# Kernel tuning notes

Measured on AMD Instinct MI355X. Metric: run time of the kernel, lower is better.

Reference implementation:

```python
import jax, jax.numpy as jnp
import numpy as np

B, S, D = 8, 512, 256          # batch, seq_len, input_depth
E, H = 8, 4                    # num_experts, num_heads
DK = DV = DO = 256             # total_key/value/output depth (per expert)
DH = DK // H                   # head dim = 64
SCALE = DH ** -0.5


def setup_inputs() -> dict:
    key = jax.random.key(0)
    ks = jax.random.split(key, 8)
    queries = jax.random.normal(ks[0], (B, S, D), jnp.float32)
    keys = jax.random.normal(ks[1], (B, S, D), jnp.float32)
    values = jax.random.normal(ks[2], (B, S, D), jnp.float32)
    mask = jax.random.randint(ks[3], (B, S, S), 0, 2).astype(bool)
    s = 0.05
    Wq = jax.random.normal(ks[4], (D, DK * E), jnp.float32) * s
    Wk = jax.random.normal(ks[5], (D, DK * E), jnp.float32) * s
    Wv = jax.random.normal(ks[6], (D, DV * E), jnp.float32) * s
    Wo = jax.random.normal(ks[7], (DV, DO * E), jnp.float32) * s
    return {"queries": queries, "keys": keys, "values": values, "mask": mask,
            "Wq": Wq, "Wk": Wk, "Wv": Wv, "Wo": Wo}


def _split_heads(x):
    # [B, S, E*H*DH] -> [B, E, H, S, DH]
    b, s, _ = x.shape
    return x.reshape(b, s, E, H, -1).transpose(0, 2, 3, 1, 4)


def reference(queries, keys, values, mask, Wq, Wk, Wv, Wo):
    q = _split_heads(queries @ Wq) * SCALE   # [B,E,H,S,DH]
    k = _split_heads(keys @ Wk)
    v = _split_heads(values @ Wv)
    logits = jnp.einsum('behqd,behkd->behqk', q, k)      # [B,E,H,S,S]
    m = mask[:, None, None].astype(jnp.float32)          # [B,1,1,S,S]
    logits = logits * (1.0 - m) + (-1e18) * m
    w = jax.nn.softmax(logits, axis=-1)
    ctx = jnp.einsum('behqk,behkd->behqd', w, v)         # [B,E,H,S,DH]
    # merge heads -> [B, S, E, H*DH]
    ctx = ctx.transpose(0, 3, 1, 2, 4).reshape(B, S, E, H * DH)
    # faithful quirk: Dense applied on rank-4 tensor -> [B,S,E,DO*E]
    return ctx @ Wo
```

## Files before the change

### kernel.cpp

```cpp
#include <hip/hip_runtime.h>
#include <stdint.h>


typedef __bf16 bf16x8 __attribute__((ext_vector_type(8)));
typedef float f32x4 __attribute__((ext_vector_type(4)));
typedef unsigned short u16x8 __attribute__((ext_vector_type(8)));
typedef unsigned short u16x4 __attribute__((ext_vector_type(4)));

#define MFMA16(a, b, c) __builtin_amdgcn_mfma_f32_16x16x32_bf16(a, b, c, 0, 0, 0)

__device__ __forceinline__ unsigned short f2bf(float x) {
    uint32_t u = __builtin_bit_cast(uint32_t, x);
    u += 0x7FFFu + ((u >> 16) & 1u);
    return (unsigned short)(u >> 16);
}

__global__ __launch_bounds__(256) void prep_kern(
        const float* __restrict__ q, const float* __restrict__ k,
        const float* __restrict__ v, const int* __restrict__ mask,
        const float* __restrict__ Wq, const float* __restrict__ Wk,
        const float* __restrict__ Wv, const float* __restrict__ Wo,
        unsigned short* __restrict__ qb, unsigned short* __restrict__ kb,
        unsigned short* __restrict__ vb, unsigned short* __restrict__ wt,
        uint32_t* __restrict__ maskbits) {
    __shared__ float tile[32][33];
    const int x = blockIdx.x, t = threadIdx.x;
    if (x < 3072) {
        int which = x >> 10;
        const float* s = (which == 0) ? q : (which == 1) ? k : v;
        unsigned short* o = (which == 0) ? qb : (which == 1) ? kb : vb;
        int i = ((x & 1023) * 256 + t) * 4;
        float4 f = *(const float4*)&s[i];
        u16x4 r;
        r[0] = f2bf(f.x); r[1] = f2bf(f.y); r[2] = f2bf(f.z); r[3] = f2bf(f.w);
        *(u16x4*)&o[i] = r;
    } else if (x < 5120) {
        int y = x - 3072;
        int wsel = y >> 9;
        const float* W = (wsel == 0) ? Wq : (wsel == 1) ? Wk : (wsel == 2) ? Wv : Wo;
        unsigned short* T = wt + wsel * 2048 * 256;
        int rem = y & 511;
        int c0 = (rem & 63) * 32, r0 = (rem >> 6) * 32;
        int tr = t >> 3, tc = (t & 7) * 4;
        float4 f = *(const float4*)&W[(r0 + tr) * 2048 + c0 + tc];
        tile[tr][tc + 0] = f.x; tile[tr][tc + 1] = f.y;
        tile[tr][tc + 2] = f.z; tile[tr][tc + 3] = f.w;
        __syncthreads();
        u16x4 o;
        o[0] = f2bf(tile[tc + 0][tr]); o[1] = f2bf(tile[tc + 1][tr]);
        o[2] = f2bf(tile[tc + 2][tr]); o[3] = f2bf(tile[tc + 3][tr]);
        *(u16x4*)&T[(c0 + tr) * 256 + r0 + tc] = o;
    } else {
        int wdx = (x - 5120) * 256 + t;
        int b = wdx >> 13, kt = (wdx >> 9) & 15, row = wdx & 511;
        const int4* mp = (const int4*)(mask + ((size_t)(b * 512 + row)) * 512 + kt * 32);
        uint32_t word = 0;
#pragma unroll
        for (int j = 0; j < 8; ++j) {
            int4 m4 = mp[j];
            word |= (uint32_t)(m4.x != 0) << (j * 4 + 0);
            word |= (uint32_t)(m4.y != 0) << (j * 4 + 1);
            word |= (uint32_t)(m4.z != 0) << (j * 4 + 2);
            word |= (uint32_t)(m4.w != 0) << (j * 4 + 3);
        }
        maskbits[wdx] = word;
    }
}

__global__ __launch_bounds__(512) void fused_kern(
        const unsigned short* __restrict__ actq,
        const unsigned short* __restrict__ actk,
        const unsigned short* __restrict__ actv,
        const unsigned short* __restrict__ Wt,
        const uint32_t* __restrict__ maskbits,
        unsigned short* __restrict__ CTX) {
    __shared__ unsigned short Klds[512 * 64];
    __shared__ unsigned short Vt[64 * 512];
    __shared__ unsigned short R3[64 * 128];
    const int bid = (int)blockIdx.x;
    const int flat = (bid & 7) * 32 + (bid >> 3);
    const int b = flat >> 5, eh = flat & 31;
    const int e = eh >> 2, h = eh & 3;
    const int t = threadIdx.x, w = t >> 6, l = t & 63, li = l & 15, g = l >> 4;
    const int tw0 = w * 64;
    const size_t actoff = (size_t)b * 512 * 256;
    const size_t wso = ((size_t)(e * 256 + h * 64)) * 256;

    bf16x8 qf[4][2];

    for (int p = 0; p < 3; ++p) {
        const unsigned short* A = ((p == 0) ? actq : (p == 1) ? actk : actv) + actoff;
        const unsigned short* W = Wt + (size_t)p * 2048 * 256 + wso;
        f32x4 acc[4][4];
#pragma unroll
        for (int m = 0; m < 4; ++m)
#pragma unroll
            for (int n = 0; n < 4; ++n) acc[m][n] = (f32x4){0.f, 0.f, 0.f, 0.f};
        for (int kh = 0; kh < 2; ++kh) {
            __syncthreads();
#pragma unroll
            for (int j = 0; j < 2; ++j) {
                int c = t + j * 512;
                int nr = c >> 4, k8 = (c & 15) * 8;
                *(u16x8*)&R3[nr * 128 + (k8 ^ ((nr & 7) << 3))] =
                    *(const u16x8*)&W[(size_t)nr * 256 + kh * 128 + k8];
            }
            __syncthreads();
#pragma unroll
            for (int kk = 0; kk < 4; ++kk) {
                const int k0 = kh * 128 + kk * 32;
                bf16x8 af[4], bfr[4];
#pragma unroll
                for (int m = 0; m < 4; ++m)
                    af[m] = *(const bf16x8*)&A[(size_t)(tw0 + m * 16 + li) * 256 + k0 + g * 8];
#pragma unroll
                for (int n = 0; n < 4; ++n) {
                    int nr = n * 16 + li;
                    bfr[n] = *(const bf16x8*)&R3[nr * 128 + ((kk * 32 + g * 8) ^ ((nr & 7) << 3))];
                }
                if (p == 2) {
#pragma unroll
                    for (int m = 0; m < 4; ++m)
#pragma unroll
                        for (int n = 0; n < 4; ++n)
                            acc[m][n] = MFMA16(af[m], bfr[n], acc[m][n]);
                } else {
#pragma unroll
                    for (int m = 0; m < 4; ++m)
#pragma unroll
                        for (int n = 0; n < 4; ++n)
                            acc[m][n] = MFMA16(bfr[n], af[m], acc[m][n]);
                }
            }
        }
        if (p == 0) {
            unsigned short* qs = Klds + w * 4096;
#pragma unroll
            for (int m = 0; m < 4; ++m)
#pragma unroll
                for (int n = 0; n < 4; ++n) {
                    int row = m * 16 + li, dh = n * 16 + g * 4;
                    u16x4 o;
#pragma unroll
                    for (int i = 0; i < 4; ++i) o[i] = f2bf(acc[m][n][i] * 0.125f);
                    *(u16x4*)&qs[row * 64 + (dh ^ ((row & 7) << 3))] = o;
                }
#pragma unroll
            for (int m = 0; m < 4; ++m) {
                int row = m * 16 + li;
                qf[m][0] = *(const bf16x8*)&qs[row * 64 + ((g * 8) ^ ((row & 7) << 3))];
                qf[m][1] = *(const bf16x8*)&qs[row * 64 + ((32 + g * 8) ^ ((row & 7) << 3))];
            }
        } else if (p == 1) {
#pragma unroll
            for (int m = 0; m < 4; ++m)
#pragma unroll
                for (int n = 0; n < 4; ++n) {
                    int tok = tw0 + m * 16 + li, dh = n * 16 + g * 4;
                    u16x4 o;
#pragma unroll
                    for (int i = 0; i < 4; ++i) o[i] = f2bf(acc[m][n][i]);
                    *(u16x4*)&Klds[tok * 64 + (dh ^ (((tok >> 1) & 7) << 3))] = o;
                }
        } else {
#pragma unroll
            for (int m = 0; m < 4; ++m)
#pragma unroll
                for (int n = 0; n < 4; ++n) {
                    int tok = tw0 + m * 16 + g * 4, dh = n * 16 + li;
                    u16x4 o;
#pragma unroll
                    for (int i = 0; i < 4; ++i) o[i] = f2bf(acc[m][n][i]);
                    *(u16x4*)&Vt[dh * 512 + (tok ^ ((dh & 7) << 3))] = o;
                }
        }
    }
    __syncthreads();

    bf16x8 vaug;
#pragma unroll
    for (int j = 0; j < 8; ++j) vaug[j] = (li == 0) ? (__bf16)1.0f : (__bf16)0.0f;
    f32x4 atc[4][4], lacc[4];
#pragma unroll
    for (int m = 0; m < 4; ++m) {
#pragma unroll
        for (int c = 0; c < 4; ++c) atc[m][c] = (f32x4){0.f, 0.f, 0.f, 0.f};
        lacc[m] = (f32x4){0.f, 0.f, 0.f, 0.f};
    }
    unsigned short* Pw = R3 + w * 1024;

    for (int kt = 0; kt < 16; ++kt) {
        bf16x8 kf[2][2];
#pragma unroll
        for (int f = 0; f < 2; ++f) {
            int tok = kt * 32 + 2 * li + f;
            const unsigned short* kr = &Klds[tok * 64];
            int sw = ((tok >> 1) & 7) << 3;
            kf[f][0] = *(const bf16x8*)&kr[(g * 8) ^ sw];
            kf[f][1] = *(const bf16x8*)&kr[(32 + g * 8) ^ sw];
        }
        f32x4 s[4][2];
#pragma unroll
        for (int m = 0; m < 4; ++m)
#pragma unroll
            for (int f = 0; f < 2; ++f) {
                f32x4 zz = (f32x4){0.f, 0.f, 0.f, 0.f};
                zz = MFMA16(qf[m][0], kf[f][0], zz);
                zz = MFMA16(qf[m][1], kf[f][1], zz);
                s[m][f] = zz;
            }
#pragma unroll
        for (int m = 0; m < 4; ++m) {
            const uint4 mw = *(const uint4*)&maskbits[(size_t)(b * 16 + kt) * 512 +
                                                      w * 64 + m * 16 + g * 4];
#pragma unroll
            for (int i = 0; i < 4; ++i) {
                uint32_t word = (i == 0) ? mw.x : (i == 1) ? mw.y : (i == 2) ? mw.z : mw.w;
                uint32_t pair = (word >> (2 * li)) & 3u;
                if (pair & 1u) s[m][0][i] = -20.f;
                if (pair & 2u) s[m][1][i] = -20.f;
            }
        }
        bf16x8 bv[4];
#pragma unroll
        for (int c = 0; c < 4; ++c) {
            int dh = c * 16 + li;
            bv[c] = *(const bf16x8*)&Vt[dh * 512 + ((kt * 32 + g * 8) ^ ((dh & 7) << 3))];
        }
#pragma unroll
        for (int mh = 0; mh < 2; ++mh) {
#pragma unroll
            for (int mm = 0; mm < 2; ++mm) {
                int m = mh * 2 + mm;
#pragma unroll
                for (int i = 0; i < 4; ++i) {
                    int row = mm * 16 + g * 4 + i;
                    uint32_t pk = (uint32_t)f2bf(__expf(s[m][0][i])) |
                                  ((uint32_t)f2bf(__expf(s[m][1][i])) << 16);
                    *(uint32_t*)&Pw[row * 32 + ((2 * li) ^ ((row & 3) << 3))] = pk;
                }
            }
#pragma unroll
            for (int mm = 0; mm < 2; ++mm) {
                int m = mh * 2 + mm;
                int rm = mm * 16 + li;
                bf16x8 pa = *(const bf16x8*)&Pw[rm * 32 + ((g * 8) ^ ((rm & 3) << 3))];
#pragma unroll
                for (int c = 0; c < 4; ++c)
                    atc[m][c] = MFMA16(bv[c], pa, atc[m][c]);
                lacc[m] = MFMA16(vaug, pa, lacc[m]);
            }
        }
    }
#pragma unroll
    for (int m = 0; m < 4; ++m) {
        float l_i = __shfl(lacc[m][0], l & 15, 64);
        float inv = 1.0f / l_i;
        const int qrow = w * 64 + m * 16 + li;
#pragma unroll
        for (int c = 0; c < 4; ++c) {
            u16x4 o;
#pragma unroll
            for (int i = 0; i < 4; ++i) o[i] = f2bf(atc[m][c][i] * inv);
            *(u16x4*)&CTX[(size_t)((b * 512 + qrow) * 8 + e) * 256 +
                          h * 64 + c * 16 + g * 4] = o;
        }
    }
}

__global__ __launch_bounds__(256) void gemm_kern(
        const unsigned short* __restrict__ A,
        const unsigned short* __restrict__ Bt,
        float* __restrict__ C, int cpx) {
    __shared__ unsigned short Asl[128 * 72];
    __shared__ unsigned short Bsl[128 * 72];
    const int bid = (int)blockIdx.x;
    const int logical = (bid & 7) * cpx + (bid >> 3);
    const int bx = logical & 15;
    const int by = logical >> 4;
    const int t = threadIdx.x, l = t & 63, w = t >> 6;
    const int li = l & 15, g = l >> 4;
    const int wr = w >> 1, wc = w & 1;
    const int rowA = by * 128, colB = bx * 128;
    f32x4 acc[4][4];
#pragma unroll
    for (int m = 0; m < 4; ++m)
#pragma unroll
        for (int n = 0; n < 4; ++n) acc[m][n] = (f32x4){0.f, 0.f, 0.f, 0.f};

    for (int kk = 0; kk < 4; ++kk) {
#pragma unroll
        for (int j = 0; j < 4; ++j) {
            int chunk = t + j * 256;
            int row = chunk >> 3, c8 = (chunk & 7) * 8;
            *(u16x8*)&Asl[row * 72 + c8] =
                *(const u16x8*)&A[(size_t)(rowA + row) * 256 + kk * 64 + c8];
            *(u16x8*)&Bsl[row * 72 + c8] =
                *(const u16x8*)&Bt[(size_t)(colB + row) * 256 + kk * 64 + c8];
        }
        __syncthreads();
#pragma unroll
        for (int hh = 0; hh < 2; ++hh) {
            bf16x8 af[4], bfr[4];
#pragma unroll
            for (int m = 0; m < 4; ++m)
                af[m] = *(const bf16x8*)&Asl[(wr * 64 + m * 16 + li) * 72 + hh * 32 + g * 8];
#pragma unroll
            for (int n = 0; n < 4; ++n)
                bfr[n] = *(const bf16x8*)&Bsl[(wc * 64 + n * 16 + li) * 72 + hh * 32 + g * 8];
#pragma unroll
            for (int m = 0; m < 4; ++m)
#pragma unroll
                for (int n = 0; n < 4; ++n)
                    acc[m][n] = MFMA16(bfr[n], af[m], acc[m][n]);
        }
        __syncthreads();
    }
#pragma unroll
    for (int m = 0; m < 4; ++m) {
        const int r = rowA + wr * 64 + m * 16 + li;
#pragma unroll
        for (int n = 0; n < 4; ++n) {
            const int c = colB + wc * 64 + n * 16 + g * 4;
            __builtin_nontemporal_store(acc[m][n], (f32x4*)&C[(size_t)r * 2048 + c]);
        }
    }
}

extern "C" void kernel_launch(void* const* d_in, const int* in_sizes, int n_in,
                              void* d_out, int out_size, void* d_ws, size_t ws_size,
                              hipStream_t stream) {
    (void)in_sizes; (void)n_in; (void)out_size; (void)ws_size;
    const float* queries = (const float*)d_in[0];
    const float* keys    = (const float*)d_in[1];
    const float* values  = (const float*)d_in[2];
    const int*   mask    = (const int*)d_in[3];
    const float* Wq = (const float*)d_in[4];
    const float* Wk = (const float*)d_in[5];
    const float* Wv = (const float*)d_in[6];
    const float* Wo = (const float*)d_in[7];

    unsigned short* CTX = (unsigned short*)d_ws;
    unsigned short* Qbf = CTX + (size_t)32768 * 256;
    unsigned short* Wt  = Qbf + (size_t)3 * 4096 * 256;
    uint32_t* maskbits  = (uint32_t*)(Wt + (size_t)4 * 2048 * 256);

    prep_kern<<<dim3(5376), 256, 0, stream>>>(queries, keys, values, mask,
                                              Wq, Wk, Wv, Wo,
                                              Qbf, Qbf + 4096 * 256, Qbf + 2 * 4096 * 256,
                                              Wt, maskbits);
    fused_kern<<<dim3(256), 512, 0, stream>>>(Qbf, Qbf + 4096 * 256,
                                              Qbf + 2 * 4096 * 256,
                                              Wt, maskbits, CTX);
    gemm_kern<<<dim3(4096), 256, 0, stream>>>(CTX, Wt + (size_t)3 * 2048 * 256,
                                              (float*)d_out, 512);
}
```

Before: 162.6 us.

## Double fused attention block to 1024 threads, use exp2 softmax and hardware bf16 cast

The fused projection+attention kernel now runs 16 waves per block, each owning 32 query/token rows instead of 64. This halves per-wave accumulator state and spreads the MFMA work over more waves to improve latency hiding. Softmax now uses exp2 with log2e folded into the Q scale and the mask constant. The manual round-to-nearest bf16 conversion is replaced by the compiler's native bf16 cast. Risks are register pressure under the 1024-thread launch bound and the extra barrier cost of the larger block.

```diff
diff --git a/kernel.cpp b/kernel.cpp
--- a/kernel.cpp
+++ b/kernel.cpp
@@ -9,11 +9,13 @@
 
 #define MFMA16(a, b, c) __builtin_amdgcn_mfma_f32_16x16x32_bf16(a, b, c, 0, 0, 0)
 
-__device__ __forceinline__ unsigned short f2bf(float x) {
-    uint32_t u = __builtin_bit_cast(uint32_t, x);
-    u += 0x7FFFu + ((u >> 16) & 1u);
-    return (unsigned short)(u >> 16);
-}
+__device__ __forceinline__ unsigned short bfc(float x) {
+    __bf16 b = (__bf16)x;
+    return __builtin_bit_cast(unsigned short, b);
+}
+
+#define QSCALE 0.18033688011112042f
+#define MASKVAL -28.853900817779268f
 
 __global__ __launch_bounds__(256) void prep_kern(
         const float* __restrict__ q, const float* __restrict__ k,
@@ -32,7 +34,7 @@
         int i = ((x & 1023) * 256 + t) * 4;
         float4 f = *(const float4*)&s[i];
         u16x4 r;
-        r[0] = f2bf(f.x); r[1] = f2bf(f.y); r[2] = f2bf(f.z); r[3] = f2bf(f.w);
+        r[0] = bfc(f.x); r[1] = bfc(f.y); r[2] = bfc(f.z); r[3] = bfc(f.w);
         *(u16x4*)&o[i] = r;
     } else if (x < 5120) {
         int y = x - 3072;
@@ -47,8 +49,8 @@
         tile[tr][tc + 2] = f.z; tile[tr][tc + 3] = f.w;
         __syncthreads();
         u16x4 o;
-        o[0] = f2bf(tile[tc + 0][tr]); o[1] = f2bf(tile[tc + 1][tr]);
-        o[2] = f2bf(tile[tc + 2][tr]); o[3] = f2bf(tile[tc + 3][tr]);
+        o[0] = bfc(tile[tc + 0][tr]); o[1] = bfc(tile[tc + 1][tr]);
+        o[2] = bfc(tile[tc + 2][tr]); o[3] = bfc(tile[tc + 3][tr]);
         *(u16x4*)&T[(c0 + tr) * 256 + r0 + tc] = o;
     } else {
         int wdx = (x - 5120) * 256 + t;
@@ -67,7 +69,7 @@
     }
 }
 
-__global__ __launch_bounds__(512) void fused_kern(
+__global__ __launch_bounds__(1024) void fused_kern(
         const unsigned short* __restrict__ actq,
         const unsigned short* __restrict__ actk,
         const unsigned short* __restrict__ actv,
@@ -82,26 +84,24 @@
     const int b = flat >> 5, eh = flat & 31;
     const int e = eh >> 2, h = eh & 3;
     const int t = threadIdx.x, w = t >> 6, l = t & 63, li = l & 15, g = l >> 4;
-    const int tw0 = w * 64;
+    const int tw0 = w * 32;
     const size_t actoff = (size_t)b * 512 * 256;
     const size_t wso = ((size_t)(e * 256 + h * 64)) * 256;
 
-    bf16x8 qf[4][2];
+    bf16x8 qf[2][2];
 
     for (int p = 0; p < 3; ++p) {
         const unsigned short* A = ((p == 0) ? actq : (p == 1) ? actk : actv) + actoff;
         const unsigned short* W = Wt + (size_t)p * 2048 * 256 + wso;
-        f32x4 acc[4][4];
-#pragma unroll
-        for (int m = 0; m < 4; ++m)
+        f32x4 acc[2][4];
+#pragma unroll
+        for (int m = 0; m < 2; ++m)
 #pragma unroll
             for (int n = 0; n < 4; ++n) acc[m][n] = (f32x4){0.f, 0.f, 0.f, 0.f};
         for (int kh = 0; kh < 2; ++kh) {
             __syncthreads();
-#pragma unroll
-            for (int j = 0; j < 2; ++j) {
-                int c = t + j * 512;
-                int nr = c >> 4, k8 = (c & 15) * 8;
+            {
+                int nr = t >> 4, k8 = (t & 15) * 8;
                 *(u16x8*)&R3[nr * 128 + (k8 ^ ((nr & 7) << 3))] =
                     *(const u16x8*)&W[(size_t)nr * 256 + kh * 128 + k8];
             }
@@ -109,9 +109,9 @@
 #pragma unroll
             for (int kk = 0; kk < 4; ++kk) {
                 const int k0 = kh * 128 + kk * 32;
-                bf16x8 af[4], bfr[4];
-#pragma unroll
-                for (int m = 0; m < 4; ++m)
+                bf16x8 af[2], bfr[4];
+#pragma unroll
+                for (int m = 0; m < 2; ++m)
                     af[m] = *(const bf16x8*)&A[(size_t)(tw0 + m * 16 + li) * 256 + k0 + g * 8];
 #pragma unroll
                 for (int n = 0; n < 4; ++n) {
@@ -120,13 +120,13 @@
                 }
                 if (p == 2) {
 #pragma unroll
-                    for (int m = 0; m < 4; ++m)
+                    for (int m = 0; m < 2; ++m)
 #pragma unroll
                         for (int n = 0; n < 4; ++n)
                             acc[m][n] = MFMA16(af[m], bfr[n], acc[m][n]);
                 } else {
 #pragma unroll
-                    for (int m = 0; m < 4; ++m)
+                    for (int m = 0; m < 2; ++m)
 #pragma unroll
                         for (int n = 0; n < 4; ++n)
                             acc[m][n] = MFMA16(bfr[n], af[m], acc[m][n]);
@@ -134,43 +134,43 @@
             }
         }
         if (p == 0) {
-            unsigned short* qs = Klds + w * 4096;
-#pragma unroll
-            for (int m = 0; m < 4; ++m)
+            unsigned short* qs = Klds + w * 2048;
+#pragma unroll
+            for (int m = 0; m < 2; ++m)
 #pragma unroll
                 for (int n = 0; n < 4; ++n) {
                     int row = m * 16 + li, dh = n * 16 + g * 4;
                     u16x4 o;
 #pragma unroll
-                    for (int i = 0; i < 4; ++i) o[i] = f2bf(acc[m][n][i] * 0.125f);
+                    for (int i = 0; i < 4; ++i) o[i] = bfc(acc[m][n][i] * QSCALE);
                     *(u16x4*)&qs[row * 64 + (dh ^ ((row & 7) << 3))] = o;
                 }
 #pragma unroll
-            for (int m = 0; m < 4; ++m) {
+            for (int m = 0; m < 2; ++m) {
                 int row = m * 16 + li;
                 qf[m][0] = *(const bf16x8*)&qs[row * 64 + ((g * 8) ^ ((row & 7) << 3))];
                 qf[m][1] = *(const bf16x8*)&qs[row * 64 + ((32 + g * 8) ^ ((row & 7) << 3))];
             }
         } else if (p == 1) {
 #pragma unroll
-            for (int m = 0; m < 4; ++m)
+            for (int m = 0; m < 2; ++m)
 #pragma unroll
                 for (int n = 0; n < 4; ++n) {
                     int tok = tw0 + m * 16 + li, dh = n * 16 + g * 4;
                     u16x4 o;
 #pragma unroll
-                    for (int i = 0; i < 4; ++i) o[i] = f2bf(acc[m][n][i]);
+                    for (int i = 0; i < 4; ++i) o[i] = bfc(acc[m][n][i]);
                     *(u16x4*)&Klds[tok * 64 + (dh ^ (((tok >> 1) & 7) << 3))] = o;
                 }
         } else {
 #pragma unroll
-            for (int m = 0; m < 4; ++m)
+            for (int m = 0; m < 2; ++m)
 #pragma unroll
                 for (int n = 0; n < 4; ++n) {
                     int tok = tw0 + m * 16 + g * 4, dh = n * 16 + li;
                     u16x4 o;
 #pragma unroll
-                    for (int i = 0; i < 4; ++i) o[i] = f2bf(acc[m][n][i]);
+                    for (int i = 0; i < 4; ++i) o[i] = bfc(acc[m][n][i]);
                     *(u16x4*)&Vt[dh * 512 + (tok ^ ((dh & 7) << 3))] = o;
                 }
         }
@@ -180,14 +180,15 @@
     bf16x8 vaug;
 #pragma unroll
     for (int j = 0; j < 8; ++j) vaug[j] = (li == 0) ? (__bf16)1.0f : (__bf16)0.0f;
-    f32x4 atc[4][4], lacc[4];
-#pragma unroll
-    for (int m = 0; m < 4; ++m) {
+    f32x4 atc[2][4], lacc[2];
+#pragma unroll
+    for (int m = 0; m < 2; ++m) {
 #pragma unroll
         for (int c = 0; c < 4; ++c) atc[m][c] = (f32x4){0.f, 0.f, 0.f, 0.f};
         lacc[m] = (f32x4){0.f, 0.f, 0.f, 0.f};
     }
-    unsigned short* Pw = R3 + w * 1024;
+    unsigned short* Pw = R3 + w * 512;
+    const uint32_t* mb = maskbits + (size_t)b * 16 * 512;
 
     for (int kt = 0; kt < 16; ++kt) {
         bf16x8 kf[2][2];
@@ -199,9 +200,9 @@
             kf[f][0] = *(const bf16x8*)&kr[(g * 8) ^ sw];
             kf[f][1] = *(const bf16x8*)&kr[(32 + g * 8) ^ sw];
         }
-        f32x4 s[4][2];
-#pragma unroll
-        for (int m = 0; m < 4; ++m)
+        f32x4 s[2][2];
+#pragma unroll
+        for (int m = 0; m < 2; ++m)
 #pragma unroll
             for (int f = 0; f < 2; ++f) {
                 f32x4 zz = (f32x4){0.f, 0.f, 0.f, 0.f};
@@ -210,15 +211,15 @@
                 s[m][f] = zz;
             }
 #pragma unroll
-        for (int m = 0; m < 4; ++m) {
-            const uint4 mw = *(const uint4*)&maskbits[(size_t)(b * 16 + kt) * 512 +
-                                                      w * 64 + m * 16 + g * 4];
+        for (int m = 0; m < 2; ++m) {
+            const uint4 mw = *(const uint4*)&mb[(size_t)kt * 512 +
+                                                tw0 + m * 16 + g * 4];
 #pragma unroll
             for (int i = 0; i < 4; ++i) {
                 uint32_t word = (i == 0) ? mw.x : (i == 1) ? mw.y : (i == 2) ? mw.z : mw.w;
                 uint32_t pair = (word >> (2 * li)) & 3u;
-                if (pair & 1u) s[m][0][i] = -20.f;
-                if (pair & 2u) s[m][1][i] = -20.f;
+                if (pair & 1u) s[m][0][i] = MASKVAL;
+                if (pair & 2u) s[m][1][i] = MASKVAL;
             }
         }
         bf16x8 bv[4];
@@ -228,40 +229,31 @@
             bv[c] = *(const bf16x8*)&Vt[dh * 512 + ((kt * 32 + g * 8) ^ ((dh & 7) << 3))];
         }
 #pragma unroll
-        for (int mh = 0; mh < 2; ++mh) {
-#pragma unroll
-            for (int mm = 0; mm < 2; ++mm) {
-                int m = mh * 2 + mm;
-#pragma unroll
-                for (int i = 0; i < 4; ++i) {
-                    int row = mm * 16 + g * 4 + i;
-                    uint32_t pk = (uint32_t)f2bf(__expf(s[m][0][i])) |
-                                  ((uint32_t)f2bf(__expf(s[m][1][i])) << 16);
-                    *(uint32_t*)&Pw[row * 32 + ((2 * li) ^ ((row & 3) << 3))] = pk;
-                }
-            }
-#pragma unroll
-            for (int mm = 0; mm < 2; ++mm) {
-                int m = mh * 2 + mm;
-                int rm = mm * 16 + li;
-                bf16x8 pa = *(const bf16x8*)&Pw[rm * 32 + ((g * 8) ^ ((rm & 3) << 3))];
-#pragma unroll
-                for (int c = 0; c < 4; ++c)
-                    atc[m][c] = MFMA16(bv[c], pa, atc[m][c]);
-                lacc[m] = MFMA16(vaug, pa, lacc[m]);
-            }
-        }
-    }
-#pragma unroll
-    for (int m = 0; m < 4; ++m) {
+        for (int m = 0; m < 2; ++m) {
+#pragma unroll
+            for (int i = 0; i < 4; ++i) {
+                int row = g * 4 + i;
+                uint32_t pk = (uint32_t)bfc(__builtin_exp2f(s[m][0][i])) |
+                              ((uint32_t)bfc(__builtin_exp2f(s[m][1][i])) << 16);
+                *(uint32_t*)&Pw[row * 32 + ((2 * li) ^ ((row & 3) << 3))] = pk;
+            }
+            bf16x8 pa = *(const bf16x8*)&Pw[li * 32 + ((g * 8) ^ ((li & 3) << 3))];
+#pragma unroll
+            for (int c = 0; c < 4; ++c)
+                atc[m][c] = MFMA16(bv[c], pa, atc[m][c]);
+            lacc[m] = MFMA16(vaug, pa, lacc[m]);
+        }
+    }
+#pragma unroll
+    for (int m = 0; m < 2; ++m) {
         float l_i = __shfl(lacc[m][0], l & 15, 64);
         float inv = 1.0f / l_i;
-        const int qrow = w * 64 + m * 16 + li;
+        const int qrow = tw0 + m * 16 + li;
 #pragma unroll
         for (int c = 0; c < 4; ++c) {
             u16x4 o;
 #pragma unroll
-            for (int i = 0; i < 4; ++i) o[i] = f2bf(atc[m][c][i] * inv);
+            for (int i = 0; i < 4; ++i) o[i] = bfc(atc[m][c][i] * inv);
             *(u16x4*)&CTX[(size_t)((b * 512 + qrow) * 8 + e) * 256 +
                           h * 64 + c * 16 + g * 4] = o;
         }
@@ -349,9 +341,9 @@
                                               Wq, Wk, Wv, Wo,
                                               Qbf, Qbf + 4096 * 256, Qbf + 2 * 4096 * 256,
                                               Wt, maskbits);
-    fused_kern<<<dim3(256), 512, 0, stream>>>(Qbf, Qbf + 4096 * 256,
-                                              Qbf + 2 * 4096 * 256,
-                                              Wt, maskbits, CTX);
+    fused_kern<<<dim3(256), 1024, 0, stream>>>(Qbf, Qbf + 4096 * 256,
+                                               Qbf + 2 * 4096 * 256,
+                                               Wt, maskbits, CTX);
     gemm_kern<<<dim3(4096), 256, 0, stream>>>(CTX, Wt + (size_t)3 * 2048 * 256,
                                               (float*)d_out, 512);
 }
```

Result: no change. 162.6 us (+0.0%).
